# Performance work log

Hardware: AMD Instinct MI355X
Metric: run time of the kernel (lower is better)

## Reference

```python
import jax, jax.numpy as jnp
import numpy as np
from jax import lax

# ---- module hyperparameters (from BasePllay_05 / AdTopoLayer init) ----
H = W = 224          # size=[224,224], grid spacing 1 given lims [[223,0],[0,223]]
N = H * W
WIN = 11
T = 25               # number of landscape sample points
K_MAX = 2            # landscape depth
M0 = 0.05            # DTM mass parameter
OUT_FEATURES = 50


def _make_neighbors():
    """Precompute, for every grid point, indices of its k nearest grid points
    (sorted by distance) and the squared offset distances. Grid is regular with
    unit spacing, so neighbor offsets are shared; border indices are clipped."""
    r = WIN // 2
    dy, dx = np.mgrid[-r:r + 1, -r:r + 1]
    dy, dx = dy.ravel(), dx.ravel()
    d2 = (dy ** 2 + dx ** 2).astype(np.float32)
    order = np.argsort(d2, kind="stable")
    dy, dx, d2 = dy[order], dx[order], d2[order]
    ys, xs = np.mgrid[0:H, 0:W]
    ny = np.clip(ys.ravel()[:, None] + dy[None, :], 0, H - 1)
    nx = np.clip(xs.ravel()[:, None] + dx[None, :], 0, W - 1)
    return jnp.asarray((ny * W + nx).astype(np.int32)), jnp.asarray(d2)

NBR_IDX, NBR_D2 = _make_neighbors()  # [N,k] int32, [k] float32


def dtm(w):
    """Distance-to-measure on the pixel grid; w: [B,N] nonneg pixel weights.
    dtm(x)^2 = sum_{j in kNN up to mass m0*W} w_j d(x,x_j)^2 / (m0*W), with a
    fractional contribution from the last neighbor (kNN truncated to k=121)."""
    nw = jnp.take(w, NBR_IDX, axis=1)                  # [B,N,k] neighbor weights
    cum = jnp.cumsum(nw, axis=-1)
    bound = (M0 * jnp.sum(w, axis=1))[:, None, None]   # [B,1,1]
    part = jnp.clip(bound - (cum - nw), 0.0, nw)       # full/partial/zero masses
    dtm2 = jnp.sum(part * NBR_D2, axis=-1) / bound[..., 0]
    return jnp.sqrt(dtm2 + 1e-12)                      # [B,N]


def landscape(f):
    """H0-style persistence-landscape features of the sublevel filtration of f.
    Local minima (3x3) are births; the 3x3 neighborhood max is the (approx)
    merge/death level. Landscape lambda_k(t) = k-th largest tent value."""
    img = f.reshape(-1, H, W)
    nmin = lax.reduce_window(img, jnp.inf, lax.min, (1, 3, 3), (1, 1, 1), "SAME")
    nmax = lax.reduce_window(img, -jnp.inf, lax.max, (1, 3, 3), (1, 1, 1), "SAME")
    is_min = (img <= nmin).reshape(-1, N)              # [B,N] bool
    birth = f                                          # [B,N]
    death = nmax.reshape(-1, N)                        # [B,N]
    tmin = f.min(axis=1)
    tmax = f.max(axis=1)
    frac = jnp.linspace(0.0, 1.0, T, dtype=f.dtype)
    tseq = tmin[:, None] + (tmax - tmin)[:, None] * frac[None, :]   # [B,T]
    tent = jnp.minimum(tseq[:, :, None] - birth[:, None, :],
                       death[:, None, :] - tseq[:, :, None])        # [B,T,N]
    tent = jnp.where(is_min[:, None, :], jnp.maximum(tent, 0.0), 0.0)
    lam, _ = lax.top_k(tent, K_MAX)                    # [B,T,K_MAX]
    return lam.reshape(-1, T * K_MAX)                  # [B,50]


def topo_layer(x, Wl, bl):
    return landscape(dtm(x)) @ Wl.T + bl               # [B,out_features]


def setup_inputs() -> dict:
    key = jax.random.key(0)
    ks = jax.random.split(key, 9)
    s = 1.0 / np.sqrt(T * K_MAX)
    inp = {"input": jax.random.uniform(ks[0], (4, 3, H, W), jnp.float32)}
    for i, n in enumerate(["1", "2", "3"]):
        inp[f"W{n}"] = jax.random.uniform(ks[1 + 2 * i], (OUT_FEATURES, T * K_MAX), jnp.float32, -s, s)
        inp[f"b{n}"] = jax.random.uniform(ks[2 + 2 * i], (OUT_FEATURES,), jnp.float32, -s, s)
    sf = 1.0 / np.sqrt(3 * OUT_FEATURES)
    inp["fc_w"] = jax.random.uniform(ks[7], (7, 3 * OUT_FEATURES), jnp.float32, -sf, sf)
    inp["fc_b"] = jax.random.uniform(ks[8], (7,), jnp.float32, -sf, sf)
    return inp


def reference(input, W1, b1, W2, b2, W3, b3, fc_w, fc_b):
    B = input.shape[0]
    x1 = topo_layer(input[:, 0].reshape(B, N), W1, b1)
    x2 = topo_layer(input[:, 1].reshape(B, N), W2, b2)
    x3 = topo_layer(input[:, 2].reshape(B, N), W3, b3)
    x = jnp.concatenate([x1, x2, x3], axis=-1)         # [B, 150]
    signal = jnp.abs(lax.stop_gradient(x)).sum(axis=0) # [150]
    output = jax.nn.relu(x) @ fc_w.T + fc_b            # [B, 7]
    return output, signal
```

## Files before the change

kernel.cpp:

```cpp
#include <hip/hip_runtime.h>
#include <math.h>

#define GH 224
#define GW 224
#define GN (GH*GW)
#define NT 25
#define NG 20
#define CAP 24576
#define SEGN 16
#define SEGCAP 1536
#define TILES_X 8
#define TILES_Y 16
#define TPI (TILES_X*TILES_Y)
#define NTILES (12*TPI)
#define NSUMJ 588
#define WTW 40
#define WTH 26
#define WTN (WTW*WTH)
#define SW 30
#define SH 26

#define WS_MM   16
#define WS_CTR  784
#define WS_LAM  1024
#define WS_SUMP 1664
#define WS_LIST 4096

struct GrpTbl { int g[11][11]; float gd2[NG]; };
constexpr GrpTbl make_g() {
    GrpTbl t{};
    int n = 0;
    for (int v = 0; v <= 50; v++) {
        bool found = false;
        for (int dy = -5; dy <= 5 && !found; dy++)
            for (int dx = -5; dx <= 5 && !found; dx++)
                if (dy*dy + dx*dx == v) found = true;
        if (found) { t.gd2[n] = (float)v; n++; }
    }
    for (int dy = 0; dy < 11; dy++)
        for (int dx = 0; dx < 11; dx++) {
            int d2 = (dy-5)*(dy-5) + (dx-5)*(dx-5);
            for (int k = 0; k < NG; k++)
                if ((float)d2 == t.gd2[k]) t.g[dy][dx] = k;
        }
    return t;
}
constexpr GrpTbl TG = make_g();
__device__ __constant__ float KD2[11] = {25.f,16.f,9.f,4.f,1.f,0.f,1.f,4.f,9.f,16.f,25.f};

__global__ __launch_bounds__(256) void k_sums(const float* __restrict__ in, float* __restrict__ ws) {
    __shared__ float sh4[4];
    int j = blockIdx.x;
    if (j < 256 && threadIdx.x == 0)
        ((float4*)ws)[j] = make_float4(0.f, 0.f, 0.f, 0.f);
    int idx = j / 49, chunk = j % 49;
    int cc = idx >> 2, bb = idx & 3;
    const float4* w4 = (const float4*)(in + (size_t)(bb*3 + cc) * GN);
    float4 v = w4[chunk*256 + threadIdx.x];
    float s = v.x + v.y + v.z + v.w;
    #pragma unroll
    for (int off = 32; off; off >>= 1) s += __shfl_down(s, off);
    if ((threadIdx.x & 63) == 0) sh4[threadIdx.x >> 6] = s;
    __syncthreads();
    if (threadIdx.x == 0) ws[WS_SUMP + j] = sh4[0] + sh4[1] + sh4[2] + sh4[3];
}

__global__ __launch_bounds__(256) void k_dtm(const float* __restrict__ in, float* __restrict__ ws) {
    __shared__ float wt[WTN];
    __shared__ float S1[SH*SW], S2[SH*SW];
    __shared__ float Ft[16*32];
    __shared__ float sb[416], sd[416];
    __shared__ float smn[4], smx[4];
    __shared__ float sbound;
    __shared__ int lcnt, gbase;
    const int tid = threadIdx.x;

    int tile_id = blockIdx.x;
    int idx  = tile_id / TPI;
    int trem = tile_id % TPI;
    int tyi = trem / TILES_X, txi = trem % TILES_X;
    int gy = tyi*14, gx = txi*28;
    int cc = idx >> 2, bb = idx & 3;
    const float* w = in + (size_t)(bb*3 + cc) * GN;
    int rep = trem & 31;
    int seg = trem & 15;

    if (tid < 64) {
        float p = (tid < 49) ? ws[WS_SUMP + idx*49 + tid] : 0.f;
        #pragma unroll
        for (int off = 32; off; off >>= 1) p += __shfl_down(p, off);
        if (tid == 0) { sbound = 0.05f * p; lcnt = 0; }
    }

    int wy0 = gy - 6, wx0 = gx - 6;
    if (txi != 0 && txi != TILES_X-1) {
        for (int i = tid; i < SH*20; i += 256) {
            int r = i / 20, q = i % 20;
            int yy = wy0 + r; yy = yy < 0 ? 0 : (yy > GH-1 ? GH-1 : yy);
            ((float2*)wt)[r*20 + q] = ((const float2*)(w + yy*GW + wx0))[q];
        }
    } else {
        for (int i = tid; i < WTN; i += 256) {
            int r = i / WTW, q = i % WTW;
            int yy = wy0 + r; yy = yy < 0 ? 0 : (yy > GH-1 ? GH-1 : yy);
            int xx = wx0 + q; xx = xx < 0 ? 0 : (xx > GW-1 ? GW-1 : xx);
            wt[i] = w[yy*GW + xx];
        }
    }
    __syncthreads();

    for (int e = tid; e < SH*SW; e += 256) {
        int r = e / SW, fc = e % SW;
        int pxc = gx - 1 + fc; pxc = pxc < 0 ? 0 : (pxc > GW-1 ? GW-1 : pxc);
        const float* bp = wt + r*WTW + (pxc - wx0 - 5);
        float s1 = 0.f, s2 = 0.f;
        #pragma unroll
        for (int k = 0; k < 11; k++) {
            float v = bp[k];
            s1 += v;
            s2 = fmaf(KD2[k], v, s2);
        }
        S1[e] = s1; S2[e] = s2;
    }
    __syncthreads();

    const bool act = tid < 240;
    int fy0 = act ? tid / 30 : 0;
    int fc  = act ? tid % 30 : 0;
    float bound = sbound;
    float fv[2] = {0.f, 0.f};
    if (act) {
        int pxc = gx - 1 + fc; pxc = pxc < 0 ? 0 : (pxc > GW-1 ? GW-1 : pxc);
        int cb = pxc - wx0 - 5;
        #pragma unroll
        for (int h = 0; h < 2; h++) {
            int fy = fy0 + h*8;
            int py = gy - 1 + fy; int pyc = py < 0 ? 0 : (py > GH-1 ? GH-1 : py);
            int vb = pyc - wy0 - 5;
            float a = 0.f, b2 = 0.f, cumT = 0.f;
            #pragma unroll
            for (int k = 0; k < 11; k++) {
                float s1 = S1[(vb+k)*SW + fc];
                float s2 = S2[(vb+k)*SW + fc];
                a = fmaf(KD2[k], s1, a);
                b2 += s2;
                cumT += s1;
            }
            float acc = a + b2;
            if (bound < cumT) {
                const float* basep = wt + vb*WTW + cb;
                float cum = 0.f; acc = 0.f;
                for (int g = 0; g < NG; g++) {
                    float gs = 0.f;
                    for (int r = 0; r < 11; r++)
                        for (int c = 0; c < 11; c++)
                            if (TG.g[r][c] == g) gs += basep[r*WTW + c];
                    float v = bound - cum;
                    v = v < 0.f ? 0.f : v;
                    v = v > gs ? gs : v;
                    acc = fmaf(v, TG.gd2[g], acc);
                    cum += gs;
                }
            }
            fv[h] = sqrtf(acc / bound + 1e-12f);
            Ft[fy*32 + fc] = fv[h];
        }
    }
    float mnv = INFINITY, mxv = -INFINITY;
    if (act) { mnv = fminf(fv[0], fv[1]); mxv = fmaxf(fv[0], fv[1]); }
    #pragma unroll
    for (int off = 32; off; off >>= 1) {
        mnv = fminf(mnv, __shfl_down(mnv, off));
        mxv = fmaxf(mxv, __shfl_down(mxv, off));
    }
    if ((tid & 63) == 0) { smn[tid>>6] = mnv; smx[tid>>6] = mxv; }
    __syncthreads();
    if (tid == 0) {
        float bm = fminf(fminf(smn[0], smn[1]), fminf(smn[2], smn[3]));
        float bX = fmaxf(fmaxf(smx[0], smx[1]), fmaxf(smx[2], smx[3]));
        atomicMax((unsigned int*)&ws[WS_MM + (idx*32 + rep)*2],     ~__float_as_uint(bm));
        atomicMax((unsigned int*)&ws[WS_MM + (idx*32 + rep)*2 + 1],  __float_as_uint(bX));
    }

    if (act && fc >= 1 && fc <= 28) {
        #pragma unroll
        for (int h = 0; h < 2; h++) {
            int fy = fy0 + h*8;
            if (fy >= 1 && fy <= 14) {
                const float* Fc = Ft + (fy-1)*32 + (fc-1);
                float f = fv[h];
                float mn = f, mx = f;
                #pragma unroll
                for (int dy = 0; dy < 3; dy++)
                    #pragma unroll
                    for (int dx = 0; dx < 3; dx++) {
                        float v = Fc[dy*32 + dx];
                        mn = fminf(mn, v); mx = fmaxf(mx, v);
                    }
                if (f <= mn) {
                    int s = atomicAdd(&lcnt, 1);
                    sb[s] = f; sd[s] = mx;
                }
            }
        }
    }
    __syncthreads();
    if (tid == 0)
        gbase = atomicAdd((int*)ws + WS_CTR + idx*SEGN + seg, lcnt);
    __syncthreads();
    int n = lcnt, gb = gbase;
    float2* list = (float2*)(ws + WS_LIST) + (size_t)idx * CAP + seg * SEGCAP;
    for (int i = tid; i < n; i += 256)
        if (gb + i < SEGCAP) list[gb + i] = make_float2(sb[i], sd[i]);
}

__global__ __launch_bounds__(256) void k_top2(float* __restrict__ ws) {
    __shared__ float r0s[4], r1s[4];
    __shared__ float s_tm[2];
    const int tid = threadIdx.x;
    int jb = blockIdx.x;
    int idx = jb / NT, t = jb % NT;

    int nmv[SEGN];
    #pragma unroll
    for (int s = 0; s < SEGN; s++) {
        int nm = ((const int*)ws)[WS_CTR + idx*SEGN + s];
        nmv[s] = nm < SEGCAP ? nm : SEGCAP;
    }

    if (tid < 32) {
        unsigned mn = ((const unsigned*)ws)[WS_MM + (idx*32 + tid)*2];
        unsigned mx = ((const unsigned*)ws)[WS_MM + (idx*32 + tid)*2 + 1];
        #pragma unroll
        for (int off = 16; off; off >>= 1) {
            unsigned m2 = __shfl_down(mn, off);
            unsigned x2 = __shfl_down(mx, off);
            mn = mn > m2 ? mn : m2;
            mx = mx > x2 ? mx : x2;
        }
        if (tid == 0) { s_tm[0] = __uint_as_float(~mn); s_tm[1] = __uint_as_float(mx); }
    }
    __syncthreads();
    float tmin = s_tm[0], tmax = s_tm[1];
    float tss = tmin + (tmax - tmin) * ((float)t / 24.0f);

    int off[SEGN+1];
    off[0] = 0;
    #pragma unroll
    for (int s = 0; s < SEGN; s++) off[s+1] = off[s] + nmv[s];
    int total = off[SEGN];
    const float2* base = (const float2*)(ws + WS_LIST) + (size_t)idx * CAP;

    float a0 = 0.f, a1 = 0.f;
    for (int g = tid; g < total; g += 256) {
        int a = g;
        #pragma unroll
        for (int s = 1; s < SEGN; s++)
            a = (g >= off[s]) ? (g - off[s] + s*SEGCAP) : a;
        float2 p = base[a];
        float v = fmaxf(fminf(tss - p.x, p.y - tss), 0.f);
        float n0 = fmaxf(a0, v);
        a1 = fmaxf(a1, fminf(a0, v));
        a0 = n0;
    }
    #pragma unroll
    for (int off2 = 32; off2; off2 >>= 1) {
        float b0 = __shfl_down(a0, off2);
        float b1 = __shfl_down(a1, off2);
        float n0 = fmaxf(a0, b0);
        a1 = fmaxf(fminf(a0, b0), fmaxf(a1, b1));
        a0 = n0;
    }
    if ((tid & 63) == 0) { r0s[tid>>6] = a0; r1s[tid>>6] = a1; }
    __syncthreads();
    if (tid == 0) {
        float c0 = r0s[0], c1 = r1s[0];
        #pragma unroll
        for (int wv = 1; wv < 4; wv++) {
            float b0 = r0s[wv], b1 = r1s[wv];
            float n0 = fmaxf(c0, b0);
            c1 = fmaxf(fminf(c0, b0), fmaxf(c1, b1));
            c0 = n0;
        }
        ws[WS_LAM + (size_t)idx*50 + t*2    ] = c0;
        ws[WS_LAM + (size_t)idx*50 + t*2 + 1] = c1;
    }
}

__global__ __launch_bounds__(256) void k_head(
        const float* __restrict__ W1, const float* __restrict__ b1,
        const float* __restrict__ W2, const float* __restrict__ b2,
        const float* __restrict__ W3, const float* __restrict__ b3,
        const float* __restrict__ fcw, const float* __restrict__ fcb,
        const float* __restrict__ ws, float* __restrict__ out)
{
    __shared__ float lamS[600];
    __shared__ float xsh[600];
    __shared__ float Wsh[7500];
    __shared__ float fcwS[1050];
    __shared__ float bS[150];
    __shared__ float fcbS[7];
    const int tid = threadIdx.x;
    for (int i = tid; i < 600; i += 256) lamS[i] = ws[WS_LAM + i];
    for (int i = tid; i < 2500; i += 256) {
        Wsh[i]        = W1[i];
        Wsh[2500 + i] = W2[i];
        Wsh[5000 + i] = W3[i];
    }
    for (int i = tid; i < 1050; i += 256) fcwS[i] = fcw[i];
    if (tid < 50) { bS[tid] = b1[tid]; bS[50+tid] = b2[tid]; bS[100+tid] = b3[tid]; }
    if (tid < 7) fcbS[tid] = fcb[tid];
    __syncthreads();
    for (int j = tid; j < 600; j += 256) {
        int b = j / 150, r = j % 150, c = r / 50, o = r % 50;
        const float* Wc = Wsh + c*2500;
        const float* lam = lamS + (c*4 + b) * 50;
        float acc = bS[c*50 + o];
        for (int f2 = 0; f2 < 50; f2++) acc += lam[f2] * Wc[o*50 + f2];
        xsh[j] = acc;
    }
    __syncthreads();
    if (tid < 150) {
        float s = 0.f;
        for (int b = 0; b < 4; b++) s += fabsf(xsh[b*150 + tid]);
        out[28 + tid] = s;
    }
    if (tid < 28) {
        int b = tid / 7, o = tid % 7;
        float acc = fcbS[o];
        for (int j = 0; j < 150; j++) acc += fmaxf(xsh[b*150 + j], 0.f) * fcwS[o*150 + j];
        out[b*7 + o] = acc;
    }
}

extern "C" void kernel_launch(void* const* d_in, const int* in_sizes, int n_in,
                              void* d_out, int out_size, void* d_ws, size_t ws_size,
                              hipStream_t stream) {
    const float* in  = (const float*)d_in[0];
    const float* W1  = (const float*)d_in[1];
    const float* b1  = (const float*)d_in[2];
    const float* W2  = (const float*)d_in[3];
    const float* b2  = (const float*)d_in[4];
    const float* W3  = (const float*)d_in[5];
    const float* b3  = (const float*)d_in[6];
    const float* fcw = (const float*)d_in[7];
    const float* fcb = (const float*)d_in[8];
    float* ws  = (float*)d_ws;
    float* out = (float*)d_out;

    k_sums<<<NSUMJ,  256, 0, stream>>>(in, ws);
    k_dtm <<<NTILES, 256, 0, stream>>>(in, ws);
    k_top2<<<300,    256, 0, stream>>>(ws);
    k_head<<<1,      256, 0, stream>>>(W1, b1, W2, b2, W3, b3, fcw, fcb, ws, out);
}
```

Baseline: 101.6 us.

## Fuse all stages into one cooperative kernel with grid syncs

```diff
diff --git a/kernel.cpp b/kernel.cpp
--- a/kernel.cpp
+++ b/kernel.cpp
@@ -1,5 +1,8 @@
 #include <hip/hip_runtime.h>
+#include <hip/hip_cooperative_groups.h>
 #include <math.h>
+
+namespace cg = cooperative_groups;
 
 #define GH 224
 #define GW 224
@@ -19,6 +22,7 @@
 #define WTN (WTW*WTH)
 #define SW 30
 #define SH 26
+#define COOPG 768
 
 #define WS_MM   16
 #define WS_CTR  784
@@ -47,6 +51,290 @@
 }
 constexpr GrpTbl TG = make_g();
 __device__ __constant__ float KD2[11] = {25.f,16.f,9.f,4.f,1.f,0.f,1.f,4.f,9.f,16.f,25.f};
+
+struct SumSM  { float sh4[4]; };
+struct DtmSM  {
+    float wt[WTN];
+    float S1[SH*SW], S2[SH*SW];
+    float Ft[16*32];
+    float sb[416], sd[416];
+    float smn[4], smx[4];
+    float sbound;
+    int lcnt, gbase;
+};
+struct Top2SM { float r0s[4], r1s[4], s_tm[2]; };
+struct HeadSM { float lamS[600], xsh[600]; };
+union FusedSM { SumSM s; DtmSM d; Top2SM t2; HeadSM h; };
+
+__global__ __launch_bounds__(256, 3) void k_all(
+        const float* __restrict__ in,
+        const float* __restrict__ W1, const float* __restrict__ b1,
+        const float* __restrict__ W2, const float* __restrict__ b2,
+        const float* __restrict__ W3, const float* __restrict__ b3,
+        const float* __restrict__ fcw, const float* __restrict__ fcb,
+        float* __restrict__ ws, float* __restrict__ out)
+{
+    __shared__ FusedSM sm;
+    const int tid = threadIdx.x;
+    const int bid = blockIdx.x;
+    cg::grid_group grid = cg::this_grid();
+
+    if (bid < 256 && tid == 0)
+        ((float4*)ws)[bid] = make_float4(0.f, 0.f, 0.f, 0.f);
+    if (bid < NSUMJ) {
+        int idx = bid / 49, chunk = bid % 49;
+        int cc = idx >> 2, bb = idx & 3;
+        const float4* w4 = (const float4*)(in + (size_t)(bb*3 + cc) * GN);
+        float4 v = w4[chunk*256 + tid];
+        float s = v.x + v.y + v.z + v.w;
+        #pragma unroll
+        for (int off = 32; off; off >>= 1) s += __shfl_down(s, off);
+        if ((tid & 63) == 0) sm.s.sh4[tid >> 6] = s;
+        __syncthreads();
+        if (tid == 0) ws[WS_SUMP + bid] = sm.s.sh4[0] + sm.s.sh4[1] + sm.s.sh4[2] + sm.s.sh4[3];
+    }
+    grid.sync();
+
+    for (int tile_id = bid; tile_id < NTILES; tile_id += COOPG) {
+        __syncthreads();
+        DtmSM& D = sm.d;
+        int idx  = tile_id / TPI;
+        int trem = tile_id % TPI;
+        int tyi = trem / TILES_X, txi = trem % TILES_X;
+        int gy = tyi*14, gx = txi*28;
+        int cc = idx >> 2, bb = idx & 3;
+        const float* w = in + (size_t)(bb*3 + cc) * GN;
+        int rep = trem & 31;
+        int seg = trem & 15;
+
+        if (tid < 64) {
+            float p = (tid < 49) ? ws[WS_SUMP + idx*49 + tid] : 0.f;
+            #pragma unroll
+            for (int off = 32; off; off >>= 1) p += __shfl_down(p, off);
+            if (tid == 0) { D.sbound = 0.05f * p; D.lcnt = 0; }
+        }
+
+        int wy0 = gy - 6, wx0 = gx - 6;
+        if (txi != 0 && txi != TILES_X-1) {
+            for (int i = tid; i < SH*20; i += 256) {
+                int r = i / 20, q = i % 20;
+                int yy = wy0 + r; yy = yy < 0 ? 0 : (yy > GH-1 ? GH-1 : yy);
+                ((float2*)D.wt)[r*20 + q] = ((const float2*)(w + yy*GW + wx0))[q];
+            }
+        } else {
+            for (int i = tid; i < WTN; i += 256) {
+                int r = i / WTW, q = i % WTW;
+                int yy = wy0 + r; yy = yy < 0 ? 0 : (yy > GH-1 ? GH-1 : yy);
+                int xx = wx0 + q; xx = xx < 0 ? 0 : (xx > GW-1 ? GW-1 : xx);
+                D.wt[i] = w[yy*GW + xx];
+            }
+        }
+        __syncthreads();
+
+        for (int e = tid; e < SH*SW; e += 256) {
+            int r = e / SW, fc = e % SW;
+            int pxc = gx - 1 + fc; pxc = pxc < 0 ? 0 : (pxc > GW-1 ? GW-1 : pxc);
+            const float* bp = D.wt + r*WTW + (pxc - wx0 - 5);
+            float s1 = 0.f, s2 = 0.f;
+            #pragma unroll
+            for (int k = 0; k < 11; k++) {
+                float v = bp[k];
+                s1 += v;
+                s2 = fmaf(KD2[k], v, s2);
+            }
+            D.S1[e] = s1; D.S2[e] = s2;
+        }
+        __syncthreads();
+
+        const bool act = tid < 240;
+        int fy0 = act ? tid / 30 : 0;
+        int fc  = act ? tid % 30 : 0;
+        float bound = D.sbound;
+        float fv[2] = {0.f, 0.f};
+        if (act) {
+            int pxc = gx - 1 + fc; pxc = pxc < 0 ? 0 : (pxc > GW-1 ? GW-1 : pxc);
+            int cb = pxc - wx0 - 5;
+            #pragma unroll
+            for (int h = 0; h < 2; h++) {
+                int fy = fy0 + h*8;
+                int py = gy - 1 + fy; int pyc = py < 0 ? 0 : (py > GH-1 ? GH-1 : py);
+                int vb = pyc - wy0 - 5;
+                float a = 0.f, b2 = 0.f, cumT = 0.f;
+                #pragma unroll
+                for (int k = 0; k < 11; k++) {
+                    float s1 = D.S1[(vb+k)*SW + fc];
+                    float s2 = D.S2[(vb+k)*SW + fc];
+                    a = fmaf(KD2[k], s1, a);
+                    b2 += s2;
+                    cumT += s1;
+                }
+                float acc = a + b2;
+                if (bound < cumT) {
+                    const float* basep = D.wt + vb*WTW + cb;
+                    float cum = 0.f; acc = 0.f;
+                    for (int g = 0; g < NG; g++) {
+                        float gs = 0.f;
+                        for (int r = 0; r < 11; r++)
+                            for (int c = 0; c < 11; c++)
+                                if (TG.g[r][c] == g) gs += basep[r*WTW + c];
+                        float v = bound - cum;
+                        v = v < 0.f ? 0.f : v;
+                        v = v > gs ? gs : v;
+                        acc = fmaf(v, TG.gd2[g], acc);
+                        cum += gs;
+                    }
+                }
+                fv[h] = sqrtf(acc / bound + 1e-12f);
+                D.Ft[fy*32 + fc] = fv[h];
+            }
+        }
+        float mnv = INFINITY, mxv = -INFINITY;
+        if (act) { mnv = fminf(fv[0], fv[1]); mxv = fmaxf(fv[0], fv[1]); }
+        #pragma unroll
+        for (int off = 32; off; off >>= 1) {
+            mnv = fminf(mnv, __shfl_down(mnv, off));
+            mxv = fmaxf(mxv, __shfl_down(mxv, off));
+        }
+        if ((tid & 63) == 0) { D.smn[tid>>6] = mnv; D.smx[tid>>6] = mxv; }
+        __syncthreads();
+        if (tid == 0) {
+            float bm = fminf(fminf(D.smn[0], D.smn[1]), fminf(D.smn[2], D.smn[3]));
+            float bX = fmaxf(fmaxf(D.smx[0], D.smx[1]), fmaxf(D.smx[2], D.smx[3]));
+            atomicMax((unsigned int*)&ws[WS_MM + (idx*32 + rep)*2],     ~__float_as_uint(bm));
+            atomicMax((unsigned int*)&ws[WS_MM + (idx*32 + rep)*2 + 1],  __float_as_uint(bX));
+        }
+
+        if (act && fc >= 1 && fc <= 28) {
+            #pragma unroll
+            for (int h = 0; h < 2; h++) {
+                int fy = fy0 + h*8;
+                if (fy >= 1 && fy <= 14) {
+                    const float* Fc = D.Ft + (fy-1)*32 + (fc-1);
+                    float f = fv[h];
+                    float mn = f, mx = f;
+                    #pragma unroll
+                    for (int dy = 0; dy < 3; dy++)
+                        #pragma unroll
+                        for (int dx = 0; dx < 3; dx++) {
+                            float v = Fc[dy*32 + dx];
+                            mn = fminf(mn, v); mx = fmaxf(mx, v);
+                        }
+                    if (f <= mn) {
+                        int s = atomicAdd(&D.lcnt, 1);
+                        D.sb[s] = f; D.sd[s] = mx;
+                    }
+                }
+            }
+        }
+        __syncthreads();
+        if (tid == 0)
+            D.gbase = atomicAdd((int*)ws + WS_CTR + idx*SEGN + seg, D.lcnt);
+        __syncthreads();
+        int n = D.lcnt, gb = D.gbase;
+        float2* list = (float2*)(ws + WS_LIST) + (size_t)idx * CAP + seg * SEGCAP;
+        for (int i = tid; i < n; i += 256)
+            if (gb + i < SEGCAP) list[gb + i] = make_float2(D.sb[i], D.sd[i]);
+    }
+    grid.sync();
+
+    if (bid < 12*NT) {
+        Top2SM& T = sm.t2;
+        int idx = bid / NT, t = bid % NT;
+
+        int nmv[SEGN];
+        #pragma unroll
+        for (int s = 0; s < SEGN; s++) {
+            int nm = ((const int*)ws)[WS_CTR + idx*SEGN + s];
+            nmv[s] = nm < SEGCAP ? nm : SEGCAP;
+        }
+
+        if (tid < 32) {
+            unsigned mn = ((const unsigned*)ws)[WS_MM + (idx*32 + tid)*2];
+            unsigned mx = ((const unsigned*)ws)[WS_MM + (idx*32 + tid)*2 + 1];
+            #pragma unroll
+            for (int off = 16; off; off >>= 1) {
+                unsigned m2 = __shfl_down(mn, off);
+                unsigned x2 = __shfl_down(mx, off);
+                mn = mn > m2 ? mn : m2;
+                mx = mx > x2 ? mx : x2;
+            }
+            if (tid == 0) { T.s_tm[0] = __uint_as_float(~mn); T.s_tm[1] = __uint_as_float(mx); }
+        }
+        __syncthreads();
+        float tmin = T.s_tm[0], tmax = T.s_tm[1];
+        float tss = tmin + (tmax - tmin) * ((float)t / 24.0f);
+
+        int off[SEGN+1];
+        off[0] = 0;
+        #pragma unroll
+        for (int s = 0; s < SEGN; s++) off[s+1] = off[s] + nmv[s];
+        int total = off[SEGN];
+        const float2* base = (const float2*)(ws + WS_LIST) + (size_t)idx * CAP;
+
+        float a0 = 0.f, a1 = 0.f;
+        for (int g = tid; g < total; g += 256) {
+            int a = g;
+            #pragma unroll
+            for (int s = 1; s < SEGN; s++)
+                a = (g >= off[s]) ? (g - off[s] + s*SEGCAP) : a;
+            float2 p = base[a];
+            float v = fmaxf(fminf(tss - p.x, p.y - tss), 0.f);
+            float n0 = fmaxf(a0, v);
+            a1 = fmaxf(a1, fminf(a0, v));
+            a0 = n0;
+        }
+        #pragma unroll
+        for (int off2 = 32; off2; off2 >>= 1) {
+            float b0 = __shfl_down(a0, off2);
+            float b1 = __shfl_down(a1, off2);
+            float n0 = fmaxf(a0, b0);
+            a1 = fmaxf(fminf(a0, b0), fmaxf(a1, b1));
+            a0 = n0;
+        }
+        if ((tid & 63) == 0) { T.r0s[tid>>6] = a0; T.r1s[tid>>6] = a1; }
+        __syncthreads();
+        if (tid == 0) {
+            float c0 = T.r0s[0], c1 = T.r1s[0];
+            #pragma unroll
+            for (int wv = 1; wv < 4; wv++) {
+                float b0 = T.r0s[wv], b1 = T.r1s[wv];
+                float n0 = fmaxf(c0, b0);
+                c1 = fmaxf(fminf(c0, b0), fmaxf(c1, b1));
+                c0 = n0;
+            }
+            ws[WS_LAM + (size_t)idx*50 + t*2    ] = c0;
+            ws[WS_LAM + (size_t)idx*50 + t*2 + 1] = c1;
+        }
+    }
+    grid.sync();
+
+    if (bid == 0) {
+        HeadSM& H = sm.h;
+        for (int i = tid; i < 600; i += 256) H.lamS[i] = ws[WS_LAM + i];
+        __syncthreads();
+        for (int j = tid; j < 600; j += 256) {
+            int b = j / 150, r = j % 150, c = r / 50, o = r % 50;
+            const float* Wc = (c == 0) ? W1 : (c == 1) ? W2 : W3;
+            const float* bc = (c == 0) ? b1 : (c == 1) ? b2 : b3;
+            const float* lam = H.lamS + (c*4 + b) * 50;
+            float acc = bc[o];
+            for (int f2 = 0; f2 < 50; f2++) acc += lam[f2] * Wc[o*50 + f2];
+            H.xsh[j] = acc;
+        }
+        __syncthreads();
+        if (tid < 150) {
+            float s = 0.f;
+            for (int b = 0; b < 4; b++) s += fabsf(H.xsh[b*150 + tid]);
+            out[28 + tid] = s;
+        }
+        if (tid < 28) {
+            int b = tid / 7, o = tid % 7;
+            float acc = fcb[o];
+            for (int j = 0; j < 150; j++) acc += fmaxf(H.xsh[b*150 + j], 0.f) * fcw[o*150 + j];
+            out[b*7 + o] = acc;
+        }
+    }
+}
 
 __global__ __launch_bounds__(256) void k_sums(const float* __restrict__ in, float* __restrict__ ws) {
     __shared__ float sh4[4];
@@ -296,26 +584,15 @@
 {
     __shared__ float lamS[600];
     __shared__ float xsh[600];
-    __shared__ float Wsh[7500];
-    __shared__ float fcwS[1050];
-    __shared__ float bS[150];
-    __shared__ float fcbS[7];
     const int tid = threadIdx.x;
     for (int i = tid; i < 600; i += 256) lamS[i] = ws[WS_LAM + i];
-    for (int i = tid; i < 2500; i += 256) {
-        Wsh[i]        = W1[i];
-        Wsh[2500 + i] = W2[i];
-        Wsh[5000 + i] = W3[i];
-    }
-    for (int i = tid; i < 1050; i += 256) fcwS[i] = fcw[i];
-    if (tid < 50) { bS[tid] = b1[tid]; bS[50+tid] = b2[tid]; bS[100+tid] = b3[tid]; }
-    if (tid < 7) fcbS[tid] = fcb[tid];
     __syncthreads();
     for (int j = tid; j < 600; j += 256) {
         int b = j / 150, r = j % 150, c = r / 50, o = r % 50;
-        const float* Wc = Wsh + c*2500;
+        const float* Wc = (c == 0) ? W1 : (c == 1) ? W2 : W3;
+        const float* bc = (c == 0) ? b1 : (c == 1) ? b2 : b3;
         const float* lam = lamS + (c*4 + b) * 50;
-        float acc = bS[c*50 + o];
+        float acc = bc[o];
         for (int f2 = 0; f2 < 50; f2++) acc += lam[f2] * Wc[o*50 + f2];
         xsh[j] = acc;
     }
@@ -327,8 +604,8 @@
     }
     if (tid < 28) {
         int b = tid / 7, o = tid % 7;
-        float acc = fcbS[o];
-        for (int j = 0; j < 150; j++) acc += fmaxf(xsh[b*150 + j], 0.f) * fcwS[o*150 + j];
+        float acc = fcb[o];
+        for (int j = 0; j < 150; j++) acc += fmaxf(xsh[b*150 + j], 0.f) * fcw[o*150 + j];
         out[b*7 + o] = acc;
     }
 }
@@ -348,8 +625,16 @@
     float* ws  = (float*)d_ws;
     float* out = (float*)d_out;
 
-    k_sums<<<NSUMJ,  256, 0, stream>>>(in, ws);
-    k_dtm <<<NTILES, 256, 0, stream>>>(in, ws);
-    k_top2<<<300,    256, 0, stream>>>(ws);
-    k_head<<<1,      256, 0, stream>>>(W1, b1, W2, b2, W3, b3, fcw, fcb, ws, out);
+    void* args[] = { (void*)&in, (void*)&W1, (void*)&b1, (void*)&W2, (void*)&b2,
+                     (void*)&W3, (void*)&b3, (void*)&fcw, (void*)&fcb,
+                     (void*)&ws, (void*)&out };
+    hipError_t err = hipLaunchCooperativeKernel((const void*)k_all,
+                                                dim3(COOPG), dim3(256),
+                                                args, 0, stream);
+    if (err != hipSuccess) {
+        k_sums<<<NSUMJ,  256, 0, stream>>>(in, ws);
+        k_dtm <<<NTILES, 256, 0, stream>>>(in, ws);
+        k_top2<<<300,    256, 0, stream>>>(ws);
+        k_head<<<1,      256, 0, stream>>>(W1, b1, W2, b2, W3, b3, fcw, fcb, ws, out);
+    }
 }
```

Result: slower. 356.7 us (+251.1%).
